# Kernel tuning notes

Measured on AMD Instinct MI355X. Metric: run time of the kernel, lower is better.

Reference implementation:

```python
import jax, jax.numpy as jnp
import numpy as np

B, M, D = 2048, 40, 64          # batch, num fields, embedding dim
HIDDEN = [128, 128, 128]        # CIN layer sizes


def setup_inputs() -> dict:
    key = jax.random.key(0)
    kx, k0, k1, k2 = jax.random.split(key, 4)
    x = jax.random.normal(kx, (B, M, D), dtype=jnp.float32)
    # torch.rand -> uniform [0, 1)
    W0 = jax.random.uniform(k0, (M, M, HIDDEN[0]), dtype=jnp.float32)
    W1 = jax.random.uniform(k1, (M, HIDDEN[0], HIDDEN[1]), dtype=jnp.float32)
    W2 = jax.random.uniform(k2, (M, HIDDEN[1], HIDDEN[2]), dtype=jnp.float32)
    return {"x": x, "W0": W0, "W1": W1, "W2": W2}


def _cin_forward(x, Ws):
    # x: [b, m, d]. Each layer k:
    #   x_next[b, l, d] = sum_{m, h} x0[b, m, d] * x_k[b, h, d] * W_k[m, h, l]
    # which equals the torch 'bil,bjl->bjil' outer product followed by
    # 'bijk,ijl->bkl' + transpose, but expressed as one fused contraction
    # (opt_einsum picks a path avoiding the worst intermediate).
    ps = []
    xk = x  # [b, H_k, d], H_0 = m
    for W in Ws:
        x_next = jnp.einsum('bmd,bhd,mhl->bld', x, xk, W)  # [b, L_k, d]
        ps.append(jnp.sum(x_next, axis=2))                  # [b, L_k]
        xk = x_next
    return jnp.concatenate(ps, axis=1)                      # [b, sum(L_k)]


def reference(x, W0, W1, W2):
    return _cin_forward(x, (W0, W1, W2))
```

## Files before the change

kernel.cpp:

```cpp
#include <hip/hip_runtime.h>
#include <hip/hip_bf16.h>
#include <cstdint>

#define BATCH 2048
#define MF    40
#define DDIM  64
#define LDIM  128
#define ROWS  (BATCH * DDIM)

typedef __attribute__((ext_vector_type(4)))  short    short4_t;
typedef __attribute__((ext_vector_type(8)))  short    short8;
typedef __attribute__((ext_vector_type(8)))  __bf16   bf16x8;
typedef __attribute__((ext_vector_type(2)))  float    floatx2;
typedef __attribute__((ext_vector_type(4)))  float    floatx4;
typedef __attribute__((ext_vector_type(16))) float    floatx16;


__device__ __forceinline__ unsigned short f32_to_bf16(float f) {
    union { float f; uint32_t u; } v; v.f = f;
    uint32_t u = v.u;
    uint32_t r = (u + 0x7fffu + ((u >> 16) & 1u)) >> 16;
    return (unsigned short)r;
}

__device__ __forceinline__ void barrier_raw() {
    asm volatile("s_barrier" ::: "memory");
}
__device__ __forceinline__ void lgkmwait0() {
    asm volatile("s_waitcnt lgkmcnt(0)" ::: "memory");
}
template <int N> __device__ __forceinline__ void vmwait() {
    if constexpr (N == 0)  asm volatile("s_waitcnt vmcnt(0)"  ::: "memory");
    if constexpr (N == 4)  asm volatile("s_waitcnt vmcnt(4)"  ::: "memory");
    if constexpr (N == 6)  asm volatile("s_waitcnt vmcnt(6)"  ::: "memory");
    if constexpr (N == 10) asm volatile("s_waitcnt vmcnt(10)" ::: "memory");
}

__global__ __launch_bounds__(256) void k_wprep_all(
    const float* __restrict__ W0, const float* __restrict__ W1,
    const float* __restrict__ W2,
    unsigned short* __restrict__ W0t,
    unsigned short* __restrict__ W1t,
    unsigned short* __restrict__ W2t) {
    __shared__ unsigned short t16[16 * 128];

    int bi = blockIdx.x;
    const float* W; unsigned short* Wt; int KK, H;
    if (bi < 160)      { W = W0; Wt = W0t; KK = 4; H = 40; }
    else if (bi < 480) { bi -= 160; W = W1; Wt = W1t; KK = 8; H = 128; }
    else               { bi -= 480; W = W2; Wt = W2t; KK = 8; H = 128; }
    const int tid = threadIdx.x;
    const int kk = bi % KK, m = bi / KK;

#pragma unroll
    for (int half = 0; half < 2; ++half) {
        const int idx = half * 1024 + tid * 4;
        const int hl  = idx >> 7, l = idx & 127;
        const int hg  = kk * 16 + hl;
        floatx4 v = {0.f, 0.f, 0.f, 0.f};
        if (hg < H)
            v = __builtin_nontemporal_load(
                (const floatx4*)&W[((size_t)m * H + hg) * LDIM + l]);
        unsigned short o[4];
        o[0] = f32_to_bf16(v.x); o[1] = f32_to_bf16(v.y);
        o[2] = f32_to_bf16(v.z); o[3] = f32_to_bf16(v.w);
        *(short4_t*)&t16[idx] = *(const short4_t*)o;
    }
    __syncthreads();

    const int lane = tid & 63, cb = tid >> 6;
    const int l  = cb * 32 + (lane & 31);
    const int hb = (lane >> 5) * 8;
    unsigned short o[8];
#pragma unroll
    for (int j = 0; j < 8; ++j) o[j] = t16[(hb + j) * 128 + l];
    *(short8*)(Wt + (((size_t)(m * KK + kk) * 4 + cb) * 64 + lane) * 8) =
        *(const short8*)o;
}

template <int KK>
__device__ __forceinline__ void layer_loop(
    const unsigned short* __restrict__ Wt,
    const float* __restrict__ x, int b,
    int lane, int hf, int r31, int cbg0, int cbg1,
    unsigned short* slabf,
    bf16x8 (&xk)[2][8], floatx16 (&acc)[2][2])
{
    constexpr int UPM  = KK / 4;
    constexpr int NU   = MF * UPM;
    constexpr int GATE = (KK == 8) ? 10 : 6;

    auto stage = [&](int uu) {
        int u = uu < NU ? uu : NU - 1;
        const unsigned short* src = Wt + (size_t)u * 8192;
        const int tid = threadIdx.x;
#pragma unroll
        for (int it = 0; it < 4; ++it) {
            int c = it * 256 + tid;
            __builtin_amdgcn_global_load_lds(
                (const __attribute__((address_space(1))) uint32_t*)(src + (size_t)c * 8),
                (__attribute__((address_space(3))) uint32_t*)(&slabf[(size_t)(u & 3) * 8192 + (size_t)c * 8]),
                16, 0, 0);
        }
    };
    auto ldfrag = [&](int u, int frag, int cb) {
        return __builtin_bit_cast(bf16x8, *(const short8*)(
            &slabf[(size_t)(u & 3) * 8192 + ((size_t)(frag * 4 + cb) * 64 + lane) * 8]));
    };

    acc[0][0] = floatx16{}; acc[0][1] = floatx16{};
    acc[1][0] = floatx16{}; acc[1][1] = floatx16{};

    vmwait<0>();
    stage(0); stage(1); stage(2);
    vmwait<4>();
    barrier_raw();

    bf16x8 bbuf[2][2];
#pragma unroll
    for (int p = 0; p < 2; ++p) {
        bbuf[p][0] = ldfrag(0, p, cbg0);
        bbuf[p][1] = ldfrag(0, p, cbg1);
    }

    float s0v = 0.f, s1v = 0.f;

#pragma unroll 1
    for (int m = 0; m < MF; ++m) {
        floatx16 P[2][2] = {};
#pragma unroll
        for (int kk = 0; kk < KK; ++kk) {
            if (kk % 4 == 0) {
                barrier_raw();
                asm volatile("s_setprio 1");
                if (kk == 0) {
                    const float* sp = x + ((size_t)b * MF + m) * DDIM + r31;
                    s0v = sp[0];
                    s1v = sp[32];
                }
                stage(m * UPM + kk / 4 + 3);
            }
            const int slot = kk & 1;
            P[0][0] = __builtin_amdgcn_mfma_f32_32x32x16_bf16(bbuf[slot][0], xk[0][kk], P[0][0], 0, 0, 0);
            P[1][0] = __builtin_amdgcn_mfma_f32_32x32x16_bf16(bbuf[slot][0], xk[1][kk], P[1][0], 0, 0, 0);
            P[0][1] = __builtin_amdgcn_mfma_f32_32x32x16_bf16(bbuf[slot][1], xk[0][kk], P[0][1], 0, 0, 0);
            P[1][1] = __builtin_amdgcn_mfma_f32_32x32x16_bf16(bbuf[slot][1], xk[1][kk], P[1][1], 0, 0, 0);
            {
                const int j  = kk + 2;
                int mm = m + ((j >= KK) ? 1 : 0);
                if (mm > MF - 1) mm = MF - 1;
                const int jj = (j >= KK) ? (j - KK) : j;
                const int u  = mm * UPM + jj / 4;
                bbuf[slot][0] = ldfrag(u, jj % 4, cbg0);
                bbuf[slot][1] = ldfrag(u, jj % 4, cbg1);
            }
            if (kk % 4 == 3) vmwait<GATE>();
        }
        asm volatile("s_setprio 0");
#pragma unroll
        for (int t = 0; t < 2; ++t) {
            const float sv = (t == 0) ? s0v : s1v;
            floatx2 s2 = {sv, sv};
#pragma unroll
            for (int cbp = 0; cbp < 2; ++cbp) {
                floatx2*       A = (floatx2*)&acc[t][cbp];
                const floatx2* Q = (const floatx2*)&P[t][cbp];
#pragma unroll
                for (int i = 0; i < 8; ++i) A[i] += s2 * Q[i];
            }
        }
    }
}

__global__ __launch_bounds__(256, 2) void k_cin(
    const float* __restrict__ x,
    const unsigned short* __restrict__ W0t,
    const unsigned short* __restrict__ W1t,
    const unsigned short* __restrict__ W2t,
    float* __restrict__ out)
{
    __shared__ unsigned short slab[4][8192];
    unsigned short* slabf = &slab[0][0];

    const int tid  = threadIdx.x;
    const int lane = tid & 63, wave = tid >> 6;
    const int hf   = lane >> 5, r31 = lane & 31;
    const int rowhalf = wave >> 1, colhalf = wave & 1;
    const int b = blockIdx.x * 2 + rowhalf;
    const int cbg0 = colhalf * 2, cbg1 = colhalf * 2 + 1;

    bf16x8   xk[2][8];
    floatx16 acc[2][2];

    auto write_ps = [&](int OFF) {
#pragma unroll
        for (int cbp = 0; cbp < 2; ++cbp) {
#pragma unroll
            for (int j = 0; j < 16; ++j) {
                float v = acc[0][cbp][j] + acc[1][cbp][j];
                v += __shfl_xor(v, 16);
                v += __shfl_xor(v, 8);
                v += __shfl_xor(v, 4);
                v += __shfl_xor(v, 2);
                v += __shfl_xor(v, 1);
                if (r31 == 0)
                    out[(size_t)b * 384 + OFF + (colhalf * 2 + cbp) * 32 +
                        (j & 3) + 8 * (j >> 2) + 4 * hf] = v;
            }
        }
    };

    auto exchange = [&]() {
        vmwait<0>();
        barrier_raw();
#pragma unroll
        for (int t = 0; t < 2; ++t)
#pragma unroll
            for (int cbp = 0; cbp < 2; ++cbp)
#pragma unroll
                for (int g = 0; g < 4; ++g) {
                    unsigned short o[4];
#pragma unroll
                    for (int i = 0; i < 4; ++i) o[i] = f32_to_bf16(acc[t][cbp][g * 4 + i]);
                    const int kk  = colhalf * 4 + cbp * 2 + (g >> 1);
                    const int hfr = g & 1;
                    *(short4_t*)(&slabf[(size_t)rowhalf * 8192 +
                        ((size_t)(t * 8 + kk) * 64 + hfr * 32 + r31) * 8 + 4 * hf]) =
                        *(const short4_t*)o;
                }
        lgkmwait0();
        barrier_raw();
#pragma unroll
        for (int t = 0; t < 2; ++t)
#pragma unroll
            for (int kk = 0; kk < 8; ++kk)
                xk[t][kk] = __builtin_bit_cast(bf16x8, *(const short8*)(
                    &slabf[(size_t)rowhalf * 8192 + ((size_t)(t * 8 + kk) * 64 + lane) * 8]));
        lgkmwait0();
        barrier_raw();
    };

#pragma unroll
    for (int t = 0; t < 2; ++t)
#pragma unroll
        for (int kk = 0; kk < 4; ++kk) {
            unsigned short tmp[8];
#pragma unroll
            for (int j = 0; j < 8; ++j) {
                int h = kk * 16 + hf * 8 + j;
                float v = (h < MF) ? x[((size_t)b * MF + h) * DDIM + t * 32 + r31] : 0.f;
                tmp[j] = f32_to_bf16(v);
            }
            xk[t][kk] = __builtin_bit_cast(bf16x8, *(const short8*)tmp);
        }

    layer_loop<4>(W0t, x, b, lane, hf, r31, cbg0, cbg1, slabf, xk, acc);
    write_ps(0);
    exchange();

    layer_loop<8>(W1t, x, b, lane, hf, r31, cbg0, cbg1, slabf, xk, acc);
    write_ps(128);
    exchange();

    layer_loop<8>(W2t, x, b, lane, hf, r31, cbg0, cbg1, slabf, xk, acc);
    write_ps(256);
}

extern "C" void kernel_launch(void* const* d_in, const int* in_sizes, int n_in,
                              void* d_out, int out_size, void* d_ws, size_t ws_size,
                              hipStream_t stream) {
    const float* x  = (const float*)d_in[0];
    const float* W0 = (const float*)d_in[1];
    const float* W1 = (const float*)d_in[2];
    const float* W2 = (const float*)d_in[3];
    float* out = (float*)d_out;

    char* ws = (char*)d_ws;
    size_t off = 0;
    auto alloc = [&](size_t bytes) -> void* {
        void* p = ws + off;
        off += (bytes + 255) & ~(size_t)255;
        return p;
    };
    unsigned short* W0t = (unsigned short*)alloc((size_t)MF * 4 * 2048 * 2);
    unsigned short* W1t = (unsigned short*)alloc((size_t)MF * 8 * 2048 * 2);
    unsigned short* W2t = (unsigned short*)alloc((size_t)MF * 8 * 2048 * 2);

    k_wprep_all<<<800, 256, 0, stream>>>(W0, W1, W2, W0t, W1t, W2t);
    k_cin<<<ROWS / 128, 256, 0, stream>>>(x, W0t, W1t, W2t, out);
}
```

Measured before the change: 450.7 us.

## Restructure weight-slab pipeline to stage two slabs per barrier period

The main loop now walks periods of two weight slabs instead of one field at a time. Each period issues one barrier and stages two slabs ahead into a 4-slot LDS ring, with explicit slot indices and vmcnt gates placed at fixed points inside the period. For the first layer, where each slab covers half a field, two fields are processed per period. The goal is to cut the number of barriers per layer and give loads more lead time, at the cost of a more complex slot and wait schedule that is easy to get wrong.

Measured after the change: 432.9 us. 3.9% less time.

```diff
diff --git a/kernel.cpp b/kernel.cpp
--- a/kernel.cpp
+++ b/kernel.cpp
@@ -32,8 +32,8 @@
 template <int N> __device__ __forceinline__ void vmwait() {
     if constexpr (N == 0)  asm volatile("s_waitcnt vmcnt(0)"  ::: "memory");
     if constexpr (N == 4)  asm volatile("s_waitcnt vmcnt(4)"  ::: "memory");
-    if constexpr (N == 6)  asm volatile("s_waitcnt vmcnt(6)"  ::: "memory");
     if constexpr (N == 10) asm volatile("s_waitcnt vmcnt(10)" ::: "memory");
+    if constexpr (N == 12) asm volatile("s_waitcnt vmcnt(12)" ::: "memory");
 }
 
 __global__ __launch_bounds__(256) void k_wprep_all(
@@ -86,11 +86,13 @@
     unsigned short* slabf,
     bf16x8 (&xk)[2][8], floatx16 (&acc)[2][2])
 {
-    constexpr int UPM  = KK / 4;
-    constexpr int NU   = MF * UPM;
-    constexpr int GATE = (KK == 8) ? 10 : 6;
-
-    auto stage = [&](int uu) {
+    constexpr int UPM = KK / 4;
+    constexpr int MPP = 2 / UPM;
+    constexpr int NU  = MF * UPM;
+    constexpr int NP  = NU / 2;
+    constexpr int G1  = 8 + 2 * MPP;
+
+    auto stage = [&](int uu, int slot) {
         int u = uu < NU ? uu : NU - 1;
         const unsigned short* src = Wt + (size_t)u * 8192;
         const int tid = threadIdx.x;
@@ -99,74 +101,79 @@
             int c = it * 256 + tid;
             __builtin_amdgcn_global_load_lds(
                 (const __attribute__((address_space(1))) uint32_t*)(src + (size_t)c * 8),
-                (__attribute__((address_space(3))) uint32_t*)(&slabf[(size_t)(u & 3) * 8192 + (size_t)c * 8]),
+                (__attribute__((address_space(3))) uint32_t*)(&slabf[(size_t)slot * 8192 + (size_t)c * 8]),
                 16, 0, 0);
         }
     };
-    auto ldfrag = [&](int u, int frag, int cb) {
+    auto ldfrag = [&](int slot, int frag, int cb) {
         return __builtin_bit_cast(bf16x8, *(const short8*)(
-            &slabf[(size_t)(u & 3) * 8192 + ((size_t)(frag * 4 + cb) * 64 + lane) * 8]));
+            &slabf[(size_t)slot * 8192 + ((size_t)(frag * 4 + cb) * 64 + lane) * 8]));
     };
 
     acc[0][0] = floatx16{}; acc[0][1] = floatx16{};
     acc[1][0] = floatx16{}; acc[1][1] = floatx16{};
 
     vmwait<0>();
-    stage(0); stage(1); stage(2);
-    vmwait<4>();
+    stage(0, 0); stage(1, 1);
+    vmwait<0>();
     barrier_raw();
 
     bf16x8 bbuf[2][2];
 #pragma unroll
-    for (int p = 0; p < 2; ++p) {
-        bbuf[p][0] = ldfrag(0, p, cbg0);
-        bbuf[p][1] = ldfrag(0, p, cbg1);
+    for (int pfr = 0; pfr < 2; ++pfr) {
+        bbuf[pfr][0] = ldfrag(0, pfr, cbg0);
+        bbuf[pfr][1] = ldfrag(0, pfr, cbg1);
     }
 
-    float s0v = 0.f, s1v = 0.f;
-
 #pragma unroll 1
-    for (int m = 0; m < MF; ++m) {
-        floatx16 P[2][2] = {};
-#pragma unroll
-        for (int kk = 0; kk < KK; ++kk) {
-            if (kk % 4 == 0) {
-                barrier_raw();
-                asm volatile("s_setprio 1");
-                if (kk == 0) {
-                    const float* sp = x + ((size_t)b * MF + m) * DDIM + r31;
-                    s0v = sp[0];
-                    s1v = sp[32];
+    for (int p = 0; p < NP; ++p) {
+        const int base = (2 * p) & 3;
+        float s0v[MPP], s1v[MPP];
+
+        barrier_raw();
+        asm volatile("s_setprio 1");
+#pragma unroll
+        for (int mi = 0; mi < MPP; ++mi) {
+            const float* sp = x + ((size_t)b * MF + (p * MPP + mi)) * DDIM + r31;
+            s0v[mi] = sp[0];
+            s1v[mi] = sp[32];
+        }
+        stage(2 * p + 2, (base + 2) & 3);
+        stage(2 * p + 3, (base + 3) & 3);
+
+#pragma unroll
+        for (int mi = 0; mi < MPP; ++mi) {
+            floatx16 P[2][2] = {};
+#pragma unroll
+            for (int kl = 0; kl < KK; ++kl) {
+                const int pkk  = mi * KK + kl;
+                const int slot = pkk & 1;
+                P[0][0] = __builtin_amdgcn_mfma_f32_32x32x16_bf16(bbuf[slot][0], xk[0][kl], P[0][0], 0, 0, 0);
+                P[1][0] = __builtin_amdgcn_mfma_f32_32x32x16_bf16(bbuf[slot][0], xk[1][kl], P[1][0], 0, 0, 0);
+                P[0][1] = __builtin_amdgcn_mfma_f32_32x32x16_bf16(bbuf[slot][1], xk[0][kl], P[0][1], 0, 0, 0);
+                P[1][1] = __builtin_amdgcn_mfma_f32_32x32x16_bf16(bbuf[slot][1], xk[1][kl], P[1][1], 0, 0, 0);
+                {
+                    const int f  = (pkk + 2) & 3;
+                    const int uo = (pkk + 2) >> 2;
+                    const int sb = (base + uo) & 3;
+                    bbuf[slot][0] = ldfrag(sb, f, cbg0);
+                    bbuf[slot][1] = ldfrag(sb, f, cbg1);
                 }
-                stage(m * UPM + kk / 4 + 3);
-            }
-            const int slot = kk & 1;
-            P[0][0] = __builtin_amdgcn_mfma_f32_32x32x16_bf16(bbuf[slot][0], xk[0][kk], P[0][0], 0, 0, 0);
-            P[1][0] = __builtin_amdgcn_mfma_f32_32x32x16_bf16(bbuf[slot][0], xk[1][kk], P[1][0], 0, 0, 0);
-            P[0][1] = __builtin_amdgcn_mfma_f32_32x32x16_bf16(bbuf[slot][1], xk[0][kk], P[0][1], 0, 0, 0);
-            P[1][1] = __builtin_amdgcn_mfma_f32_32x32x16_bf16(bbuf[slot][1], xk[1][kk], P[1][1], 0, 0, 0);
-            {
-                const int j  = kk + 2;
-                int mm = m + ((j >= KK) ? 1 : 0);
-                if (mm > MF - 1) mm = MF - 1;
-                const int jj = (j >= KK) ? (j - KK) : j;
-                const int u  = mm * UPM + jj / 4;
-                bbuf[slot][0] = ldfrag(u, jj % 4, cbg0);
-                bbuf[slot][1] = ldfrag(u, jj % 4, cbg1);
-            }
-            if (kk % 4 == 3) vmwait<GATE>();
-        }
-        asm volatile("s_setprio 0");
-#pragma unroll
-        for (int t = 0; t < 2; ++t) {
-            const float sv = (t == 0) ? s0v : s1v;
-            floatx2 s2 = {sv, sv};
-#pragma unroll
-            for (int cbp = 0; cbp < 2; ++cbp) {
-                floatx2*       A = (floatx2*)&acc[t][cbp];
-                const floatx2* Q = (const floatx2*)&P[t][cbp];
-#pragma unroll
-                for (int i = 0; i < 8; ++i) A[i] += s2 * Q[i];
+                if (pkk == 1) vmwait<G1>();
+                if (pkk == 5) vmwait<4>();
+            }
+            if (mi == MPP - 1) asm volatile("s_setprio 0");
+#pragma unroll
+            for (int t = 0; t < 2; ++t) {
+                const float sv = (t == 0) ? s0v[mi] : s1v[mi];
+                floatx2 s2 = {sv, sv};
+#pragma unroll
+                for (int cbp = 0; cbp < 2; ++cbp) {
+                    floatx2*       A = (floatx2*)&acc[t][cbp];
+                    const floatx2* Q = (const floatx2*)&P[t][cbp];
+#pragma unroll
+                    for (int i = 0; i < 8; ++i) A[i] += s2 * Q[i];
+                }
             }
         }
     }
```
